# Performance work log

Measured on AMD Instinct MI355X. Metric: run time of the kernel, lower is better.

## Reference

```python
import jax, jax.numpy as jnp
import numpy as np

B, M, D = 512, 96, 512
H = 8            # num_heads
DH = D // H      # head dim
NC = 3           # num_clusters
BETA = 5
MEM = 1024       # memory_size
EPS = 1e-8


def _l2norm(x, axis=-1):
    # torch F.cosine_similarity clamps each norm at eps=1e-8
    n = jnp.linalg.norm(x, axis=axis, keepdims=True)
    return x / jnp.maximum(n, EPS)


def _dynamic_clustering(sims):
    # sims: (B, M). Sort descending, split into NC equal groups,
    # per-group mean and (unbiased) std. (dynamic_clustering is not
    # defined in the source repo; this is the assumed implementation.)
    s = -jnp.sort(-sims, axis=1)               # descending
    g = s.reshape(B, NC, M // NC)
    means = g.mean(axis=-1)                    # (B, NC)
    stds = jnp.std(g, axis=-1, ddof=1)         # (B, NC)
    return means, stds


def setup_inputs() -> dict:
    key = jax.random.key(0)
    ks = jax.random.split(key, 6)
    vis_global = jax.random.normal(ks[0], (B, D), dtype=jnp.float32)
    text_features = jax.random.normal(ks[1], (B, M, D), dtype=jnp.float32)
    scale = 1.0 / np.sqrt(D)
    in_proj_w = jax.random.normal(ks[2], (3 * D, D), dtype=jnp.float32) * scale
    in_proj_b = jnp.zeros((3 * D,), dtype=jnp.float32)
    out_proj_w = jax.random.normal(ks[3], (D, D), dtype=jnp.float32) * scale
    out_proj_b = jnp.zeros((D,), dtype=jnp.float32)
    text_memory = jax.random.normal(ks[4], (MEM, D), dtype=jnp.float32)
    tau_p_log = jnp.log(jnp.asarray(0.1, dtype=jnp.float32))
    tau_n_log = jnp.log(jnp.asarray(0.05, dtype=jnp.float32))
    return dict(vis_global=vis_global, text_features=text_features,
                in_proj_w=in_proj_w, in_proj_b=in_proj_b,
                out_proj_w=out_proj_w, out_proj_b=out_proj_b,
                text_memory=text_memory, tau_p_log=tau_p_log, tau_n_log=tau_n_log)


def reference(vis_global, text_features, in_proj_w, in_proj_b,
              out_proj_w, out_proj_b, text_memory, tau_p_log, tau_n_log):
    # --- dynamic clustering over visual-text cosine sims ---
    sims = jnp.einsum('bd,bmd->bm', _l2norm(vis_global), _l2norm(text_features))
    means, stds = _dynamic_clustering(sims)
    cluster_scores = means / (stds + 1e-6)     # (B, NC)

    # --- MultiheadAttention: 1-token query, M-token key/value ---
    wq, wk, wv = in_proj_w[:D], in_proj_w[D:2 * D], in_proj_w[2 * D:]
    bq, bk, bv = in_proj_b[:D], in_proj_b[D:2 * D], in_proj_b[2 * D:]
    q = (vis_global @ wq.T + bq).reshape(B, H, DH)              # (B,H,DH)
    k = (text_features @ wk.T + bk).reshape(B, M, H, DH)        # (B,M,H,DH)
    v = (text_features @ wv.T + bv).reshape(B, M, H, DH)
    attn = jax.nn.softmax(jnp.einsum('bhd,bmhd->bhm', q, k) / np.sqrt(DH), axis=-1)
    ctx = jnp.einsum('bhm,bmhd->bhd', attn, v).reshape(B, D)
    corrected = ctx @ out_proj_w.T + out_proj_b                 # (B, D)

    tau_p = jnp.exp(tau_p_log)
    tau_n = jnp.exp(tau_n_log)
    pos_sim = jnp.sum(_l2norm(vis_global) * _l2norm(corrected), axis=-1)  # (B,)

    # memory-bank scatter (ptr starts at 0) + negatives, all detached
    corr_sg = jax.lax.stop_gradient(corrected)
    mem = text_memory.at[0:B].set(corr_sg)
    all_negs = jnp.concatenate([jnp.roll(corr_sg, 1, axis=0), mem], axis=0)  # (B+MEM, D)

    neg_sims = _l2norm(vis_global) @ _l2norm(all_negs).T        # (B, B+MEM)
    hard_negs, _ = jax.lax.top_k(neg_sims, BETA)                # (B, BETA)

    pos_term = jnp.exp(pos_sim / tau_p)
    neg_terms = jnp.exp(hard_negs / tau_n).sum(axis=1)
    loss = -jnp.mean(jnp.log(pos_term / (pos_term + neg_terms + 1e-8)))
    return loss, corrected, cluster_scores
```

## Files before the change

### kernel.cpp

```cpp
#include <hip/hip_runtime.h>
#include <math.h>

typedef unsigned short u16;
typedef unsigned int u32;
typedef __attribute__((ext_vector_type(8))) short short8;
typedef __attribute__((ext_vector_type(8))) _Float16 half8;
typedef __attribute__((ext_vector_type(4))) float f32x4;

#define EPS 1e-8f

__device__ inline float bf2f(u16 u) {
    union { u32 i; float f; } v; v.i = ((u32)u) << 16; return v.f;
}
__device__ inline u16 f2bf(float f) {
    union { float f; u32 u; } v; v.f = f;
    u32 r = v.u + 0x7fffu + ((v.u >> 16) & 1u);
    return (u16)(r >> 16);
}
__device__ inline u16 f2h(float f) {
    _Float16 h = (_Float16)f;
    union { _Float16 hh; u16 u; } v; v.hh = h; return v.u;
}
__device__ inline u32 pack2(float a, float b) {
    return (u32)f2bf(a) | ((u32)f2bf(b) << 16);
}
__device__ inline float wave_sum(float v) {
    for (int off = 32; off; off >>= 1) v += __shfl_xor(v, off, 64);
    return v;
}

__device__ __forceinline__ void stage64x512(const u16* __restrict__ Ag, size_t lda,
                                            u16* __restrict__ As) {
    const int t = threadIdx.x;
    const int srow = t >> 2;
    const int c0 = (t & 3) * 8;
    #pragma unroll
    for (int kk = 0; kk < 16; kk++) {
        int c = c0 + kk * 32;
        *(uint4*)&As[srow * 520 + c] = *(const uint4*)&Ag[(size_t)srow * lda + c];
    }
}
__device__ __forceinline__ void mfma_k512(const u16* __restrict__ As,
                                          const u16* __restrict__ Bs,
                                          f32x4 (&acc)[2][2]) {
    const int t = threadIdx.x, lane = t & 63, w = t >> 6;
    const int wm = (w >> 1) * 32, wn = (w & 1) * 32;
    const int l16 = lane & 15, quad = lane >> 4;
    #pragma unroll
    for (int ks = 0; ks < 16; ks++) {
        short8 af[2], bfr[2];
        #pragma unroll
        for (int i = 0; i < 2; i++)
            af[i] = *(const short8*)&As[(wm + i * 16 + l16) * 520 + ks * 32 + quad * 8];
        #pragma unroll
        for (int j = 0; j < 2; j++)
            bfr[j] = *(const short8*)&Bs[(wn + j * 16 + l16) * 520 + ks * 32 + quad * 8];
        #pragma unroll
        for (int i = 0; i < 2; i++)
            #pragma unroll
            for (int j = 0; j < 2; j++)
                acc[i][j] = __builtin_amdgcn_mfma_f32_16x16x32_bf16(af[i], bfr[j], acc[i][j], 0, 0, 0);
    }
}

__global__ __launch_bounds__(256) void prep(const float* __restrict__ vis,
                                            const float* __restrict__ ipw,
                                            const float* __restrict__ opw,
                                            const float* __restrict__ tm,
                                            float* __restrict__ vis_n,
                                            u16* __restrict__ vis_nb,
                                            u16* __restrict__ vis_b,
                                            u16* __restrict__ wqb,
                                            u16* __restrict__ wvb,
                                            u16* __restrict__ wob,
                                            u16* __restrict__ negsb,
                                            u16* __restrict__ wkT,
                                            u16* __restrict__ woT,
                                            float* __restrict__ corrSS,
                                            float* __restrict__ loss0)
{
    int bid = blockIdx.x;
    int t = threadIdx.x;
    if (bid >= 1088) {
        __shared__ __align__(16) u16 T[64 * 72];
        int idx = bid - 1088;
        int a = idx >> 3, cb = idx & 7;
        int r = t >> 2, c0 = (t & 3) * 16;
        #pragma unroll
        for (int q = 0; q < 4; q++) {
            float4 v = *(const float4*)&opw[(size_t)(a * 64 + r) * 512 + cb * 64 + c0 + q * 4];
            T[(c0 + q * 4 + 0) * 72 + r] = f2bf(v.x);
            T[(c0 + q * 4 + 1) * 72 + r] = f2bf(v.y);
            T[(c0 + q * 4 + 2) * 72 + r] = f2bf(v.z);
            T[(c0 + q * 4 + 3) * 72 + r] = f2bf(v.w);
        }
        __syncthreads();
        int j = t >> 2, ch = (t & 3) * 16;
        *(uint4*)&woT[(size_t)(cb * 64 + j) * 512 + a * 64 + ch]     = *(const uint4*)&T[j * 72 + ch];
        *(uint4*)&woT[(size_t)(cb * 64 + j) * 512 + a * 64 + ch + 8] = *(const uint4*)&T[j * 72 + ch + 8];
        return;
    }
    if (bid >= 1024) {
        __shared__ __align__(16) u16 T[64 * 72];
        int idx = bid - 1024;
        int a = idx >> 3, cb = idx & 7;
        const float* wk = ipw + 262144;
        int r = t >> 2, c0 = (t & 3) * 16;
        #pragma unroll
        for (int q = 0; q < 4; q++) {
            float4 v = *(const float4*)&wk[(size_t)(a * 64 + r) * 512 + cb * 64 + c0 + q * 4];
            T[(c0 + q * 4 + 0) * 72 + r] = f2h(v.x);
            T[(c0 + q * 4 + 1) * 72 + r] = f2h(v.y);
            T[(c0 + q * 4 + 2) * 72 + r] = f2h(v.z);
            T[(c0 + q * 4 + 3) * 72 + r] = f2h(v.w);
        }
        __syncthreads();
        int j = t >> 2, ch = (t & 3) * 16;
        *(uint4*)&wkT[(size_t)(cb * 64 + j) * 512 + a * 64 + ch]     = *(const uint4*)&T[j * 72 + ch];
        *(uint4*)&wkT[(size_t)(cb * 64 + j) * 512 + a * 64 + ch + 8] = *(const uint4*)&T[j * 72 + ch + 8];
        return;
    }
    if (bid >= 896) {
        int wave = t >> 6, lane = t & 63;
        int j = 512 + (bid - 896) * 4 + wave;
        const float* row = tm + (size_t)(j - 512) * 512 + lane * 8;
        float4 x0 = *(const float4*)row;
        float4 x1 = *(const float4*)(row + 4);
        float ss = x0.x*x0.x + x0.y*x0.y + x0.z*x0.z + x0.w*x0.w
                 + x1.x*x1.x + x1.y*x1.y + x1.z*x1.z + x1.w*x1.w;
        ss = wave_sum(ss);
        float inv = 1.0f / fmaxf(sqrtf(ss), EPS);
        uint4 pk;
        pk.x = pack2(x0.x*inv, x0.y*inv); pk.y = pack2(x0.z*inv, x0.w*inv);
        pk.z = pack2(x1.x*inv, x1.y*inv); pk.w = pack2(x1.z*inv, x1.w*inv);
        *(uint4*)(negsb + (size_t)j * 512 + lane * 8) = pk;
        return;
    }
    if (bid >= 128) {
        int i = ((bid - 128) * 256 + t) * 4;
        const float* src; u16* dst; int j;
        if (i < 262144)      { j = i;          src = ipw + j;          dst = wqb + j; }
        else if (i < 524288) { j = i - 262144; src = ipw + 524288 + j; dst = wvb + j; }
        else                 { j = i - 524288; src = opw + j;          dst = wob + j; }
        float4 v = *(const float4*)src;
        uint2 pk; pk.x = pack2(v.x, v.y); pk.y = pack2(v.z, v.w);
        *(uint2*)dst = pk;
        return;
    }
    if (bid == 0) {
        if (t == 0) loss0[0] = 0.0f;
        corrSS[t] = 0.0f;
        corrSS[t + 256] = 0.0f;
    }
    int wave = t >> 6, lane = t & 63;
    int b = bid * 4 + wave;
    const float* row = vis + (size_t)b * 512 + lane * 8;
    float4 x0 = *(const float4*)row;
    float4 x1 = *(const float4*)(row + 4);
    uint4 rk;
    rk.x = pack2(x0.x, x0.y); rk.y = pack2(x0.z, x0.w);
    rk.z = pack2(x1.x, x1.y); rk.w = pack2(x1.z, x1.w);
    *(uint4*)(vis_b + (size_t)b * 512 + lane * 8) = rk;
    float ss = x0.x*x0.x + x0.y*x0.y + x0.z*x0.z + x0.w*x0.w
             + x1.x*x1.x + x1.y*x1.y + x1.z*x1.z + x1.w*x1.w;
    ss = wave_sum(ss);
    float inv = 1.0f / fmaxf(sqrtf(ss), EPS);
    float4 y0, y1;
    y0.x = x0.x*inv; y0.y = x0.y*inv; y0.z = x0.z*inv; y0.w = x0.w*inv;
    y1.x = x1.x*inv; y1.y = x1.y*inv; y1.z = x1.z*inv; y1.w = x1.w*inv;
    *(float4*)(vis_n + (size_t)b * 512 + lane * 8)     = y0;
    *(float4*)(vis_n + (size_t)b * 512 + lane * 8 + 4) = y1;
    uint4 pk;
    pk.x = pack2(y0.x, y0.y); pk.y = pack2(y0.z, y0.w);
    pk.z = pack2(y1.x, y1.y); pk.w = pack2(y1.z, y1.w);
    *(uint4*)(vis_nb + (size_t)b * 512 + lane * 8) = pk;
}

__global__ __launch_bounds__(256) void mid(const u16* __restrict__ visb,
                                           const u16* __restrict__ vis_nb,
                                           const u16* __restrict__ wqb,
                                           const float* __restrict__ ipb,
                                           const u16* __restrict__ wkT,
                                           u16* __restrict__ qkb,
                                           const u16* __restrict__ negsb,
                                           float* __restrict__ ns,
                                           const u16* __restrict__ woT,
                                           u16* __restrict__ G,
                                           const float* __restrict__ opb,
                                           float* __restrict__ vb,
                                           const float* __restrict__ vis_n)
{
    __shared__ __align__(16) u16 SM[3 * 64 * 72];
    const int bid = blockIdx.x;
    const int t = threadIdx.x, lane = t & 63, w = t >> 6;

    if (bid >= 192) {
        int idx = bid - 192;
        #pragma unroll 2
        for (int k = 0; k < 16; k++) {
            int b = idx * 64 + w * 16 + k;
            const float* vn = vis_n + (size_t)b * 512 + lane * 8;
            float4 a = *(const float4*)vn, c = *(const float4*)(vn + 4);
            const float* bo = opb + lane * 8;
            float4 b0 = *(const float4*)bo, b1 = *(const float4*)(bo + 4);
            float dt = a.x*b0.x + a.y*b0.y + a.z*b0.z + a.w*b0.w
                     + c.x*b1.x + c.y*b1.y + c.z*b1.z + c.w*b1.w;
            dt = wave_sum(dt);
            if (lane == 0) vb[b] = dt;
        }
        return;
    }

    const int wm = (w >> 1) * 32, wn = (w & 1) * 32;
    const int l16 = lane & 15, quad = lane >> 4;
    const int srow = t >> 3, scol = (t & 7) * 8;

    if (bid >= 64) {
        u16* As = SM;
        u16* Bs = SM + 4608;
        bool isG = (bid >= 128);
        int idx = bid - (isG ? 128 : 64);
        int m0 = (idx & 7) * 64, n0 = (idx >> 3) * 64;
        const u16* Bsrc = isG ? (woT + (size_t)n0 * 512)
                              : (negsb + (size_t)(512 + n0) * 512);
        f32x4 acc[2][2];
        for (int i = 0; i < 2; i++)
            for (int j = 0; j < 2; j++)
                for (int e = 0; e < 4; e++) acc[i][j][e] = 0.f;
        for (int ko = 0; ko < 512; ko += 64) {
            __syncthreads();
            #pragma unroll
            for (int i = 0; i < 2; i++) {
                int row = i * 32 + srow;
                *(uint4*)&As[row * 72 + scol] = *(const uint4*)&vis_nb[(size_t)(m0 + row) * 512 + ko + scol];
                *(uint4*)&Bs[row * 72 + scol] = *(const uint4*)&Bsrc[(size_t)row * 512 + ko + scol];
            }
            __syncthreads();
            #pragma unroll
            for (int ks = 0; ks < 2; ks++) {
                short8 af[2], bfr[2];
                #pragma unroll
                for (int i = 0; i < 2; i++)
                    af[i] = *(const short8*)&As[(wm + i * 16 + l16) * 72 + ks * 32 + quad * 8];
                #pragma unroll
                for (int j = 0; j < 2; j++)
                    bfr[j] = *(const short8*)&Bs[(wn + j * 16 + l16) * 72 + ks * 32 + quad * 8];
                #pragma unroll
                for (int i = 0; i < 2; i++)
                    #pragma unroll
                    for (int j = 0; j < 2; j++)
                        acc[i][j] = __builtin_amdgcn_mfma_f32_16x16x32_bf16(af[i], bfr[j], acc[i][j], 0, 0, 0);
            }
        }
        #pragma unroll
        for (int i = 0; i < 2; i++)
            #pragma unroll
            for (int j = 0; j < 2; j++)
                #pragma unroll
                for (int r = 0; r < 4; r++) {
                    int row = m0 + wm + i * 16 + quad * 4 + r;
                    int col = n0 + wn + j * 16 + l16;
                    if (isG) G[(size_t)row * 512 + col] = f2bf(acc[i][j][r]);
                    else     ns[(size_t)row * 1024 + 512 + col] = acc[i][j][r];
                }
        return;
    }

    u16* As = SM;
    u16* Bs = SM + 4608;
    u16* Qf = SM + 9216;
    const int m0 = (bid & 7) * 64, h = bid >> 3;

    f32x4 acc[2][2];
    for (int i = 0; i < 2; i++)
        for (int j = 0; j < 2; j++)
            for (int e = 0; e < 4; e++) acc[i][j][e] = 0.f;

    for (int ko = 0; ko < 512; ko += 64) {
        __syncthreads();
        #pragma unroll
        for (int i = 0; i < 2; i++) {
            int row = i * 32 + srow;
            *(uint4*)&As[row * 72 + scol] = *(const uint4*)&visb[(size_t)(m0 + row) * 512 + ko + scol];
            *(uint4*)&Bs[row * 72 + scol] = *(const uint4*)&wqb[(size_t)(h * 64 + row) * 512 + ko + scol];
        }
        __syncthreads();
        #pragma unroll
        for (int ks = 0; ks < 2; ks++) {
            short8 af[2], bfr[2];
            #pragma unroll
            for (int i = 0; i < 2; i++)
                af[i] = *(const short8*)&As[(wm + i * 16 + l16) * 72 + ks * 32 + quad * 8];
            #pragma unroll
            for (int j = 0; j < 2; j++)
                bfr[j] = *(const short8*)&Bs[(wn + j * 16 + l16) * 72 + ks * 32 + quad * 8];
            #pragma unroll
            for (int i = 0; i < 2; i++)
                #pragma unroll
                for (int j = 0; j < 2; j++)
                    acc[i][j] = __builtin_amdgcn_mfma_f32_16x16x32_bf16(af[i], bfr[j], acc[i][j], 0, 0, 0);
        }
    }
    #pragma unroll
    for (int i = 0; i < 2; i++)
        #pragma unroll
        for (int j = 0; j < 2; j++)
            #pragma unroll
            for (int r = 0; r < 4; r++) {
                int rl = wm + i * 16 + quad * 4 + r;
                int cl = wn + j * 16 + l16;
                Qf[rl * 72 + cl] = f2h(acc[i][j][r] + ipb[h * 64 + cl]);
            }
    for (int jt = 0; jt < 8; jt++) {
        __syncthreads();
        #pragma unroll
        for (int i = 0; i < 2; i++) {
            int row = i * 32 + srow;
            *(uint4*)&Bs[row * 72 + scol] = *(const uint4*)&wkT[(size_t)(jt * 64 + row) * 512 + h * 64 + scol];
        }
        __syncthreads();
        f32x4 a2[2][2];
        for (int i = 0; i < 2; i++)
            for (int j = 0; j < 2; j++)
                for (int e = 0; e < 4; e++) a2[i][j][e] = 0.f;
        #pragma unroll
        for (int ks = 0; ks < 2; ks++) {
            half8 af[2], bfr[2];
            #pragma unroll
            for (int i = 0; i < 2; i++)
                af[i] = *(const half8*)&Qf[(wm + i * 16 + l16) * 72 + ks * 32 + quad * 8];
            #pragma unroll
            for (int j = 0; j < 2; j++)
                bfr[j] = *(const half8*)&Bs[(wn + j * 16 + l16) * 72 + ks * 32 + quad * 8];
            #pragma unroll
            for (int i = 0; i < 2; i++)
                #pragma unroll
                for (int j = 0; j < 2; j++)
                    a2[i][j] = __builtin_amdgcn_mfma_f32_16x16x32_f16(af[i], bfr[j], a2[i][j], 0, 0, 0);
        }
        #pragma unroll
        for (int i = 0; i < 2; i++)
            #pragma unroll
            for (int j = 0; j < 2; j++)
                #pragma unroll
                for (int r = 0; r < 4; r++) {
                    int rb = m0 + wm + i * 16 + quad * 4 + r;
                    int cj = jt * 64 + wn + j * 16 + l16;
                    qkb[((size_t)rb * 8 + h) * 512 + cj] = f2bf(a2[i][j][r]);
                }
    }
}

__global__ __launch_bounds__(1024) void attn(const float* __restrict__ tf,
                                             const float* __restrict__ vis_n,
                                             const u16* __restrict__ qkb,
                                             u16* __restrict__ u_allb,
                                             float* __restrict__ out_cs)
{
    __shared__ __align__(16) u16 Xs[96 * 520];
    __shared__ __align__(16) u16 Qs[16 * 520];
    __shared__ __align__(16) u16 Ps[16 * 104];
    __shared__ float Sc[16 * 100];
    __shared__ float sm_[96], srt[96], linv[8];

    const int b = blockIdx.x;
    const int t = threadIdx.x, w = t >> 6, lane = t & 63;
    const int l16 = lane & 15, quad = lane >> 4;

    const float4* v4 = (const float4*)(vis_n + (size_t)b * 512 + lane * 8);
    float4 va = v4[0], vbv = v4[1];

    #pragma unroll
    for (int i = 0; i < 3; i++) {
        int m0r = w + i * 32;
        int m1r = m0r + 16;
        const float4* pa = (const float4*)(tf + ((size_t)b * 96 + m0r) * 512 + lane * 8);
        const float4* pb = (const float4*)(tf + ((size_t)b * 96 + m1r) * 512 + lane * 8);
        float4 a0 = pa[0], c0 = pa[1];
        float4 a1 = pb[0], c1 = pb[1];
        float ss0 = a0.x*a0.x + a0.y*a0.y + a0.z*a0.z + a0.w*a0.w
                  + c0.x*c0.x + c0.y*c0.y + c0.z*c0.z + c0.w*c0.w;
        float dt0 = a0.x*va.x + a0.y*va.y + a0.z*va.z + a0.w*va.w
                  + c0.x*vbv.x + c0.y*vbv.y + c0.z*vbv.z + c0.w*vbv.w;
        float ss1 = a1.x*a1.x + a1.y*a1.y + a1.z*a1.z + a1.w*a1.w
                  + c1.x*c1.x + c1.y*c1.y + c1.z*c1.z + c1.w*c1.w;
        float dt1 = a1.x*va.x + a1.y*va.y + a1.z*va.z + a1.w*va.w
                  + c1.x*vbv.x + c1.y*vbv.y + c1.z*vbv.z + c1.w*vbv.w;
        #pragma unroll
        for (int off = 32; off; off >>= 1) {
            ss0 += __shfl_xor(ss0, off, 64);
            dt0 += __shfl_xor(dt0, off, 64);
            ss1 += __shfl_xor(ss1, off, 64);
            dt1 += __shfl_xor(dt1, off, 64);
        }
        if (lane == 0) {
            sm_[m0r] = dt0 / fmaxf(sqrtf(ss0), EPS);
            sm_[m1r] = dt1 / fmaxf(sqrtf(ss1), EPS);
        }
        uint4 pk0, pk1;
        pk0.x = pack2(a0.x, a0.y); pk0.y = pack2(a0.z, a0.w);
        pk0.z = pack2(c0.x, c0.y); pk0.w = pack2(c0.z, c0.w);
        pk1.x = pack2(a1.x, a1.y); pk1.y = pack2(a1.z, a1.w);
        pk1.z = pack2(c1.x, c1.y); pk1.w = pack2(c1.z, c1.w);
        *(uint4*)&Xs[m0r * 520 + lane * 8] = pk0;
        *(uint4*)&Xs[m1r * 520 + lane * 8] = pk1;
    }
    if (w < 8) {
        *(uint4*)&Qs[w * 520 + lane * 8] = *(const uint4*)(qkb + ((size_t)b * 8 + w) * 512 + lane * 8);
    } else {
        uint4 z; z.x = 0; z.y = 0; z.z = 0; z.w = 0;
        *(uint4*)&Qs[w * 520 + lane * 8] = z;
    }
    __syncthreads();

    if (w < 6) {
        f32x4 acc;
        for (int e = 0; e < 4; e++) acc[e] = 0.f;
        #pragma unroll
        for (int ks = 0; ks < 16; ks++) {
            short8 a = *(const short8*)&Xs[(w * 16 + l16) * 520 + ks * 32 + quad * 8];
            short8 q = *(const short8*)&Qs[l16 * 520 + ks * 32 + quad * 8];
            acc = __builtin_amdgcn_mfma_f32_16x16x32_bf16(a, q, acc, 0, 0, 0);
        }
        #pragma unroll
        for (int r = 0; r < 4; r++)
            Sc[l16 * 100 + w * 16 + quad * 4 + r] = acc[r] * 0.125f;
    }
    __syncthreads();

    if (w < 8) {
        float e0 = __expf(Sc[w * 100 + lane]);
        float e1 = (lane < 32) ? __expf(Sc[w * 100 + 64 + lane]) : 0.f;
        float l = wave_sum(e0 + e1);
        Ps[w * 104 + lane] = f2bf(e0);
        if (lane < 32) Ps[w * 104 + 64 + lane] = f2bf(e1);
        if (lane == 0) linv[w] = 1.0f / l;
    } else {
        Ps[w * 104 + lane] = 0;
        if (lane < 40) Ps[w * 104 + 64 + lane] = 0;
    }
    if (t < 96) {
        float v = sm_[t]; int r = 0;
        for (int j = 0; j < 96; j++) {
            float u = sm_[j];
            r += (u > v) || (u == v && j < t);
        }
        srt[r] = v;
    }
    __syncthreads();

    #pragma unroll
    for (int jj = 0; jj < 2; jj++) {
        int n0 = (w * 2 + jj) * 16;
        f32x4 acc;
        for (int e = 0; e < 4; e++) acc[e] = 0.f;
        #pragma unroll
        for (int ks = 0; ks < 3; ks++) {
            short8 ap = *(const short8*)&Ps[l16 * 104 + ks * 32 + quad * 8];
            short8 bx;
            #pragma unroll
            for (int j = 0; j < 8; j++)
                bx[j] = (short)Xs[(ks * 32 + quad * 8 + j) * 520 + n0 + l16];
            acc = __builtin_amdgcn_mfma_f32_16x16x32_bf16(ap, bx, acc, 0, 0, 0);
        }
        if (quad < 2) {
            #pragma unroll
            for (int r = 0; r < 4; r++) {
                int h = quad * 4 + r;
                u_allb[((size_t)b * 8 + h) * 512 + n0 + l16] = f2bf(acc[r] * linv[h]);
            }
        }
    }
    if (t < 3) {
        float mean = 0.f;
        #pragma unroll 8
        for (int i = 0; i < 32; i++) mean += srt[t * 32 + i];
        mean *= (1.0f / 32.0f);
        float var = 0.f;
        #pragma unroll 8
        for (int i = 0; i < 32; i++) { float d = srt[t * 32 + i] - mean; var += d * d; }
        var *= (1.0f / 31.0f);
        out_cs[b * 3 + t] = mean / (sqrtf(var) + 1e-6f);
    }
}

__global__ __launch_bounds__(256) void ghead(const u16* __restrict__ u_allb,
                                             const u16* __restrict__ wvb,
                                             const float* __restrict__ bv,
                                             u16* __restrict__ ctxb)
{
    __shared__ __align__(16) u16 As[64 * 520];
    __shared__ __align__(16) u16 Bs[64 * 520];
    const int bid = blockIdx.x;
    const int m0 = (bid & 7) * 64, h = bid >> 3;
    const int t = threadIdx.x, lane = t & 63, w = t >> 6;
    const int wm = (w >> 1) * 32, wn = (w & 1) * 32;
    const int l16 = lane & 15, quad = lane >> 4;

    f32x4 acc[2][2];
    for (int i = 0; i < 2; i++)
        for (int j = 0; j < 2; j++)
            for (int e = 0; e < 4; e++) acc[i][j][e] = 0.f;

    stage64x512(u_allb + (size_t)m0 * 4096 + (size_t)h * 512, 4096, As);
    stage64x512(wvb + (size_t)h * 64 * 512, 512, Bs);
    __syncthreads();
    mfma_k512(As, Bs, acc);

    for (int i = 0; i < 2; i++) {
        int row = m0 + wm + i * 16 + quad * 4;
        for (int j = 0; j < 2; j++) {
            int col = wn + j * 16 + l16;
            float bb = bv[h * 64 + col];
            for (int r = 0; r < 4; r++)
                ctxb[(size_t)(row + r) * 512 + h * 64 + col] = f2bf(acc[i][j][r] + bb);
        }
    }
}

__global__ __launch_bounds__(256) void tail2(const u16* __restrict__ ctxb,
                                             const u16* __restrict__ wob,
                                             const float* __restrict__ bias,
                                             float* __restrict__ Cf,
                                             float* __restrict__ corrSS,
                                             const u16* __restrict__ G,
                                             const float* __restrict__ vb,
                                             float* __restrict__ ns)
{
    __shared__ __align__(16) u16 As[64 * 520];
    __shared__ __align__(16) u16 Bs[64 * 520];
    const int bid = blockIdx.x;
    const int t = threadIdx.x, lane = t & 63, w = t >> 6;
    const int wm = (w >> 1) * 32, wn = (w & 1) * 32;
    const int l16 = lane & 15, quad = lane >> 4;

    f32x4 acc[2][2];
    for (int i = 0; i < 2; i++)
        for (int j = 0; j < 2; j++)
            for (int e = 0; e < 4; e++) acc[i][j][e] = 0.f;

    if (bid < 64) {
        const int m0 = (bid & 7) * 64, n0 = (bid >> 3) * 64;
        stage64x512(ctxb + (size_t)m0 * 512, 512, As);
        stage64x512(wob + (size_t)n0 * 512, 512, Bs);
        __syncthreads();
        mfma_k512(As, Bs, acc);
        #pragma unroll
        for (int i = 0; i < 2; i++) {
            #pragma unroll
            for (int r = 0; r < 4; r++) {
                int row = m0 + wm + i * 16 + quad * 4 + r;
                float s = 0.f;
                #pragma unroll
                for (int j = 0; j < 2; j++) {
                    int col = n0 + wn + j * 16 + l16;
                    float v = acc[i][j][r] + bias[col];
                    Cf[(size_t)row * 512 + col] = v;
                    s += v * v;
                }
                s += __shfl_xor(s, 1, 64); s += __shfl_xor(s, 2, 64);
                s += __shfl_xor(s, 4, 64); s += __shfl_xor(s, 8, 64);
                if (l16 == 0) atomicAdd(&corrSS[row], s);
            }
        }
        return;
    }

    const int idx = bid - 64;
    const int m0 = (idx & 7) * 64, n0 = (idx >> 3) * 64;
    stage64x512(G + (size_t)m0 * 512, 512, As);
    stage64x512(ctxb + (size_t)n0 * 512, 512, Bs);
    __syncthreads();
    mfma_k512(As, Bs, acc);
    for (int i = 0; i < 2; i++) {
        int row = m0 + wm + i * 16 + quad * 4;
        for (int j = 0; j < 2; j++) {
            int col = n0 + wn + j * 16 + l16;
            for (int r = 0; r < 4; r++)
                ns[(size_t)(row + r) * 1024 + col] = acc[i][j][r] + vb[row + r];
        }
    }
}

__global__ __launch_bounds__(256) void topk_loss(const float* __restrict__ ns,
                                                 const float* __restrict__ corrSS,
                                                 const float* __restrict__ tau_p_log,
                                                 const float* __restrict__ tau_n_log,
                                                 float* __restrict__ out_loss)
{
    __shared__ float invn[512];
    __shared__ float cv[20];
    __shared__ int   cjx[20];
    int b = blockIdx.x, t = threadIdx.x;
    int w = t >> 6, lane = t & 63;

    {
        float s0 = corrSS[t], s1 = corrSS[t + 256];
        invn[t]       = 1.0f / fmaxf(sqrtf(s0), EPS);
        invn[t + 256] = 1.0f / fmaxf(sqrtf(s1), EPS);
    }
    __syncthreads();

    const float4 raw = *(const float4*)(ns + (size_t)b * 1024 + t * 4);
    float lv[4] = {raw.x, raw.y, raw.z, raw.w};
    int   li[4] = {t * 4, t * 4 + 1, t * 4 + 2, t * 4 + 3};
    if (t < 128) {
        lv[0] *= invn[t * 4];     lv[1] *= invn[t * 4 + 1];
        lv[2] *= invn[t * 4 + 2]; lv[3] *= invn[t * 4 + 3];
    }
    #pragma unroll
    for (int i = 1; i < 4; i++) {
        float kv = lv[i]; int kx = li[i];
        int j = i - 1;
        #pragma unroll
        for (int k = 0; k < 3; k++) {
            if (j >= 0 && lv[j] < kv) { lv[j + 1] = lv[j]; li[j + 1] = li[j]; j--; }
        }
        lv[j + 1] = kv; li[j + 1] = kx;
    }
    int lp = 0;
    #pragma unroll
    for (int rd = 0; rd < 5; rd++) {
        float mv = (lp < 4) ? lv[lp] : -1e30f;
        int   mi = (lp < 4) ? li[lp] : 0;
        int   ml = lane;
        #pragma unroll
        for (int off = 32; off; off >>= 1) {
            float ov = __shfl_xor(mv, off, 64);
            int   oi = __shfl_xor(mi, off, 64);
            int   ol = __shfl_xor(ml, off, 64);
            if (ov > mv || (ov == mv && ol < ml)) { mv = ov; mi = oi; ml = ol; }
        }
        if (lane == ml) lp++;
        if (lane == 0) { cv[w * 5 + rd] = mv; cjx[w * 5 + rd] = mi; }
    }
    __syncthreads();
    if (w == 0) {
        float v  = (lane < 20) ? cv[lane] : -1e30f;
        int   jx = (lane < 20) ? cjx[lane] : 0;
        float tn = expf(tau_n_log[0]);
        float itn = 1.0f / tn;
        float nsum = 0.f; int coll = 0;
        #pragma unroll
        for (int rd = 0; rd < 5; rd++) {
            float mv = v; int ml = lane; int mj = jx;
            #pragma unroll
            for (int off = 32; off; off >>= 1) {
                float ov = __shfl_xor(mv, off, 64);
                int   oj = __shfl_xor(mj, off, 64);
                int   ol = __shfl_xor(ml, off, 64);
                if (ov > mv || (ov == mv && ol < ml)) { mv = ov; mj = oj; ml = ol; }
            }
            int mult = (mj < 512) ? 2 : 1;
            int take = 5 - coll;
            take = (mult < take) ? mult : take;
            if (take < 0) take = 0;
            nsum += (float)take * __expf(mv * itn);
            coll += take;
            if (lane == ml) v = -1e30f;
        }
        if (lane == 0) {
            float pos = ns[(size_t)b * 1024 + b] * invn[b];
            float tp = expf(tau_p_log[0]);
            float p = expf(pos / tp);
            float term = logf(p / (p + nsum + 1e-8f));
            atomicAdd(out_loss, -term * (1.0f / 512.0f));
        }
    }
}

extern "C" void kernel_launch(void* const* d_in, const int* in_sizes, int n_in,
                              void* d_out, int out_size, void* d_ws, size_t ws_size,
                              hipStream_t stream) {
    const float* vis = (const float*)d_in[0];
    const float* tf  = (const float*)d_in[1];
    const float* ipw = (const float*)d_in[2];
    const float* ipb = (const float*)d_in[3];
    const float* opw = (const float*)d_in[4];
    const float* opb = (const float*)d_in[5];
    const float* tm  = (const float*)d_in[6];
    const float* tpl = (const float*)d_in[7];
    const float* tnl = (const float*)d_in[8];

    float* out       = (float*)d_out;
    float* out_loss  = out;
    float* out_corr  = out + 1;
    float* out_cs    = out + 1 + 512 * 512;

    char* p = (char*)d_ws;
    auto alloc = [&](size_t bytes) { char* r = p; p += (bytes + 255) & ~(size_t)255; return r; };
    float* vis_n  = (float*)alloc(512 * 512 * 4);
    u16*   vis_nb = (u16*)  alloc(512 * 512 * 2);
    u16*   vis_b  = (u16*)  alloc(512 * 512 * 2);
    u16*   wqb    = (u16*)  alloc(512 * 512 * 2);
    u16*   wvb    = (u16*)  alloc(512 * 512 * 2);
    u16*   wob    = (u16*)  alloc(512 * 512 * 2);
    u16*   wkT    = (u16*)  alloc(512 * 512 * 2);
    u16*   woT    = (u16*)  alloc(512 * 512 * 2);
    u16*   G      = (u16*)  alloc(512 * 512 * 2);
    u16*   qkb    = (u16*)  alloc((size_t)512 * 8 * 512 * 2);
    u16*   u_allb = (u16*)  alloc((size_t)512 * 8 * 512 * 2);
    u16*   ctxb   = (u16*)  alloc(512 * 512 * 2);
    u16*   negsb  = (u16*)  alloc(1024 * 512 * 2);
    float* ns     = (float*)alloc(512 * 1024 * 4);
    float* corrSS = (float*)alloc(512 * 4);
    float* vb     = (float*)alloc(512 * 4);

    const float* bv = ipb + 2 * 512;

    prep<<<1152, 256, 0, stream>>>(vis, ipw, opw, tm, vis_n, vis_nb, vis_b,
                                   wqb, wvb, wob, negsb, wkT, woT, corrSS, out_loss);
    mid<<<200, 256, 0, stream>>>(vis_b, vis_nb, wqb, ipb, wkT, qkb, negsb, ns,
                                 woT, G, opb, vb, vis_n);
    attn<<<512, 1024, 0, stream>>>(tf, vis_n, qkb, u_allb, out_cs);
    ghead<<<64, 256, 0, stream>>>(u_allb, wvb, bv, ctxb);
    tail2<<<128, 256, 0, stream>>>(ctxb, wob, opb, out_corr, corrSS, G, vb, ns);
    topk_loss<<<512, 256, 0, stream>>>(ns, corrSS, tpl, tnl, out_loss);
}
```

Baseline: 224.6 us.

## Stage full K=512 tiles into LDS once instead of per-64 chunk loop

Measured after the change: 219.4 us (median of 2 runs). -2.3%, faster.

```diff
diff --git a/kernel.cpp b/kernel.cpp
--- a/kernel.cpp
+++ b/kernel.cpp
@@ -190,9 +190,11 @@
                                            float* __restrict__ vb,
                                            const float* __restrict__ vis_n)
 {
-    __shared__ __align__(16) u16 SM[3 * 64 * 72];
+    __shared__ __align__(16) u16 SMEM[2 * 64 * 520];
     const int bid = blockIdx.x;
     const int t = threadIdx.x, lane = t & 63, w = t >> 6;
+    const int wm = (w >> 1) * 32, wn = (w & 1) * 32;
+    const int l16 = lane & 15, quad = lane >> 4;
 
     if (bid >= 192) {
         int idx = bid - 192;
@@ -211,13 +213,10 @@
         return;
     }
 
-    const int wm = (w >> 1) * 32, wn = (w & 1) * 32;
-    const int l16 = lane & 15, quad = lane >> 4;
-    const int srow = t >> 3, scol = (t & 7) * 8;
+    u16* As = SMEM;
+    u16* Bs = SMEM + 33280;
 
     if (bid >= 64) {
-        u16* As = SM;
-        u16* Bs = SM + 4608;
         bool isG = (bid >= 128);
         int idx = bid - (isG ? 128 : 64);
         int m0 = (idx & 7) * 64, n0 = (idx >> 3) * 64;
@@ -227,31 +226,10 @@
         for (int i = 0; i < 2; i++)
             for (int j = 0; j < 2; j++)
                 for (int e = 0; e < 4; e++) acc[i][j][e] = 0.f;
-        for (int ko = 0; ko < 512; ko += 64) {
-            __syncthreads();
-            #pragma unroll
-            for (int i = 0; i < 2; i++) {
-                int row = i * 32 + srow;
-                *(uint4*)&As[row * 72 + scol] = *(const uint4*)&vis_nb[(size_t)(m0 + row) * 512 + ko + scol];
-                *(uint4*)&Bs[row * 72 + scol] = *(const uint4*)&Bsrc[(size_t)row * 512 + ko + scol];
-            }
-            __syncthreads();
-            #pragma unroll
-            for (int ks = 0; ks < 2; ks++) {
-                short8 af[2], bfr[2];
-                #pragma unroll
-                for (int i = 0; i < 2; i++)
-                    af[i] = *(const short8*)&As[(wm + i * 16 + l16) * 72 + ks * 32 + quad * 8];
-                #pragma unroll
-                for (int j = 0; j < 2; j++)
-                    bfr[j] = *(const short8*)&Bs[(wn + j * 16 + l16) * 72 + ks * 32 + quad * 8];
-                #pragma unroll
-                for (int i = 0; i < 2; i++)
-                    #pragma unroll
-                    for (int j = 0; j < 2; j++)
-                        acc[i][j] = __builtin_amdgcn_mfma_f32_16x16x32_bf16(af[i], bfr[j], acc[i][j], 0, 0, 0);
-            }
-        }
+        stage64x512(vis_nb + (size_t)m0 * 512, 512, As);
+        stage64x512(Bsrc, 512, Bs);
+        __syncthreads();
+        mfma_k512(As, Bs, acc);
         #pragma unroll
         for (int i = 0; i < 2; i++)
             #pragma unroll
@@ -266,9 +244,6 @@
         return;
     }
 
-    u16* As = SM;
-    u16* Bs = SM + 4608;
-    u16* Qf = SM + 9216;
     const int m0 = (bid & 7) * 64, h = bid >> 3;
 
     f32x4 acc[2][2];
@@ -276,31 +251,14 @@
         for (int j = 0; j < 2; j++)
             for (int e = 0; e < 4; e++) acc[i][j][e] = 0.f;
 
-    for (int ko = 0; ko < 512; ko += 64) {
-        __syncthreads();
-        #pragma unroll
-        for (int i = 0; i < 2; i++) {
-            int row = i * 32 + srow;
-            *(uint4*)&As[row * 72 + scol] = *(const uint4*)&visb[(size_t)(m0 + row) * 512 + ko + scol];
-            *(uint4*)&Bs[row * 72 + scol] = *(const uint4*)&wqb[(size_t)(h * 64 + row) * 512 + ko + scol];
-        }
-        __syncthreads();
-        #pragma unroll
-        for (int ks = 0; ks < 2; ks++) {
-            short8 af[2], bfr[2];
-            #pragma unroll
-            for (int i = 0; i < 2; i++)
-                af[i] = *(const short8*)&As[(wm + i * 16 + l16) * 72 + ks * 32 + quad * 8];
-            #pragma unroll
-            for (int j = 0; j < 2; j++)
-                bfr[j] = *(const short8*)&Bs[(wn + j * 16 + l16) * 72 + ks * 32 + quad * 8];
-            #pragma unroll
-            for (int i = 0; i < 2; i++)
-                #pragma unroll
-                for (int j = 0; j < 2; j++)
-                    acc[i][j] = __builtin_amdgcn_mfma_f32_16x16x32_bf16(af[i], bfr[j], acc[i][j], 0, 0, 0);
-        }
-    }
+    stage64x512(visb + (size_t)m0 * 512, 512, As);
+    stage64x512(wqb + (size_t)(h * 64) * 512, 512, Bs);
+    __syncthreads();
+    mfma_k512(As, Bs, acc);
+    __syncthreads();
+
+    u16* Qf = SMEM;
+    u16* Bk = SMEM + 4608;
     #pragma unroll
     for (int i = 0; i < 2; i++)
         #pragma unroll
@@ -311,14 +269,18 @@
                 int cl = wn + j * 16 + l16;
                 Qf[rl * 72 + cl] = f2h(acc[i][j][r] + ipb[h * 64 + cl]);
             }
+    {
+        int r0 = t >> 3;
+        int c0 = (t & 7) * 8;
+        #pragma unroll
+        for (int pass = 0; pass < 16; pass++) {
+            int r = pass * 32 + r0;
+            *(uint4*)&Bk[r * 72 + c0] = *(const uint4*)&wkT[(size_t)r * 512 + h * 64 + c0];
+        }
+    }
+    __syncthreads();
+
     for (int jt = 0; jt < 8; jt++) {
-        __syncthreads();
-        #pragma unroll
-        for (int i = 0; i < 2; i++) {
-            int row = i * 32 + srow;
-            *(uint4*)&Bs[row * 72 + scol] = *(const uint4*)&wkT[(size_t)(jt * 64 + row) * 512 + h * 64 + scol];
-        }
-        __syncthreads();
         f32x4 a2[2][2];
         for (int i = 0; i < 2; i++)
             for (int j = 0; j < 2; j++)
@@ -331,7 +293,7 @@
                 af[i] = *(const half8*)&Qf[(wm + i * 16 + l16) * 72 + ks * 32 + quad * 8];
             #pragma unroll
             for (int j = 0; j < 2; j++)
-                bfr[j] = *(const half8*)&Bs[(wn + j * 16 + l16) * 72 + ks * 32 + quad * 8];
+                bfr[j] = *(const half8*)&Bk[(jt * 64 + wn + j * 16 + l16) * 72 + ks * 32 + quad * 8];
             #pragma unroll
             for (int i = 0; i < 2; i++)
                 #pragma unroll
```
